# Performance work log

Measured on AMD Instinct MI355X. Metric: run time of the kernel, lower is better.

Reference implementation:

```python
import jax, jax.numpy as jnp
import numpy as np

NSITES = 64   # 2 * nphysical spin-orbital sites
BOND = 128    # MPS bond dimension D
BATCH = 16384 # sampled occupation configurations


def setup_inputs() -> dict:
    key = jax.random.key(0)
    k1, k2, k3, k4 = jax.random.split(key, 4)
    # Site tensors A[k, n] in R^{D x D}; scaled so chain products stay O(1).
    data = jax.random.normal(k1, (NSITES, 2, BOND, BOND), dtype=jnp.float32) / jnp.sqrt(jnp.float32(BOND))
    left = jax.random.normal(k2, (BOND,), dtype=jnp.float32)
    right = jax.random.normal(k3, (BOND,), dtype=jnp.float32)
    # Occupation-number vectors (0/1 per spin orbital).
    onstate = jax.random.randint(k4, (BATCH, NSITES), 0, 2, dtype=jnp.int32)
    # Orbital-ordering permutation (identity here).
    image2 = jnp.arange(NSITES, dtype=jnp.int32)
    return {"onstate": onstate, "data": data, "left": left, "right": right, "image2": image2}


def reference(onstate, data, left, right, image2):
    # Reorder physical indices per the stored orbital image: [B, NSITES]
    occ = onstate[:, image2]
    B = occ.shape[0]
    D = left.shape[0]
    v0 = jnp.broadcast_to(left, (B, D))  # left boundary, batched

    def step(v, xs):
        A, n = xs  # A: [2, D, D] site tensor, n: [B] occupations at this site
        # Contract with both quantum-number blocks, then select per sample
        # (equivalent to gathering the block indexed by the occupation).
        v_new = jnp.where((n == 1)[:, None], v @ A[1], v @ A[0])  # [B, D]
        return v_new, None

    vT, _ = jax.lax.scan(step, v0, (data, occ.T))
    return vT @ right  # amplitudes psi(n): [B]
```

## Files before the change

kernel.cpp:

```cpp
#include <hip/hip_runtime.h>
#include <hip/hip_bf16.h>

#define NS 64
#define NP 32
#define DIM 128
#define BATCH_N 16384

typedef float f32x4 __attribute__((ext_vector_type(4)));
typedef _Float16 f16x8 __attribute__((ext_vector_type(8)));
typedef __fp16 fp16x2 __attribute__((ext_vector_type(2)));
typedef unsigned int u32;
typedef unsigned long long u64;

__device__ __forceinline__ unsigned short f2h(float f) {
    _Float16 h = (_Float16)f;
    return __builtin_bit_cast(unsigned short, h);
}

__global__ __launch_bounds__(256)
void prep_pair_frags(const float* __restrict__ data,
                     unsigned short* __restrict__ afrag) {
    __shared__ float LA[2 * 32 * 129];
    __shared__ float LB[2 * 32 * 68];

    const int p   = blockIdx.x >> 3;
    const int kk  = (blockIdx.x >> 1) & 3;
    const int mh  = blockIdx.x & 1;
    const int tid = threadIdx.x;
    const int kgrp = tid >> 4;
    const int mgrp = tid & 15;

    const float* A0 = data + ((size_t)(2 * p) * 2 + 0) * DIM * DIM;
    const float* A1 = A0 + DIM * DIM;
    const float* B0 = data + ((size_t)(2 * p + 1) * 2 + 0) * DIM * DIM;
    const float* B1 = B0 + DIM * DIM;

    for (int c = tid; c < 32 * DIM; c += 256) {
        int kl = c >> 7, j = c & 127;
        float a0 = A0[(kk * 32 + kl) * DIM + j];
        float a1 = A1[(kk * 32 + kl) * DIM + j];
        LA[kl * 129 + j] = a0;
        LA[32 * 129 + kl * 129 + j] = a1 - a0;
    }

    float acc[2][2][2][4];
#pragma unroll
    for (int L = 0; L < 2; ++L)
#pragma unroll
        for (int R = 0; R < 2; ++R)
#pragma unroll
            for (int i = 0; i < 2; ++i)
#pragma unroll
                for (int mi = 0; mi < 4; ++mi) acc[L][R][i][mi] = 0.f;

    for (int ch = 0; ch < 4; ++ch) {
        __syncthreads();
        for (int c = tid; c < 32 * 64; c += 256) {
            int jl = c >> 6, ml = c & 63;
            float b0 = B0[(ch * 32 + jl) * DIM + mh * 64 + ml];
            float b1 = B1[(ch * 32 + jl) * DIM + mh * 64 + ml];
            LB[jl * 68 + ml] = b0;
            LB[32 * 68 + jl * 68 + ml] = b1 - b0;
        }
        __syncthreads();
#pragma unroll 2
        for (int jl = 0; jl < 32; ++jl) {
            int j = ch * 32 + jl;
            float la0[2], la1[2];
#pragma unroll
            for (int i = 0; i < 2; ++i) {
                la0[i] = LA[(kgrp * 2 + i) * 129 + j];
                la1[i] = LA[32 * 129 + (kgrp * 2 + i) * 129 + j];
            }
            f32x4 lb0 = *reinterpret_cast<const f32x4*>(&LB[jl * 68 + mgrp * 4]);
            f32x4 lb1 = *reinterpret_cast<const f32x4*>(&LB[32 * 68 + jl * 68 + mgrp * 4]);
#pragma unroll
            for (int i = 0; i < 2; ++i)
#pragma unroll
                for (int mi = 0; mi < 4; ++mi) {
                    acc[0][0][i][mi] += la0[i] * lb0[mi];
                    acc[1][0][i][mi] += la1[i] * lb0[mi];
                    acc[0][1][i][mi] += la0[i] * lb1[mi];
                    acc[1][1][i][mi] += la1[i] * lb1[mi];
                }
        }
    }

    const int H   = kk >> 1;
    const int kq  = kk & 1;
#pragma unroll
    for (int t = 0; t < 4; ++t) {
        int L = t & 1, R = t >> 1;
#pragma unroll
        for (int i = 0; i < 2; ++i)
#pragma unroll
            for (int mi = 0; mi < 4; ++mi) {
                int k = kk * 32 + kgrp * 2 + i;
                int m = mh * 64 + mgrp * 4 + mi;
                int mm = m >> 4;
                int lane = ((k & 31) >> 3) * 16 + (m & 15);
                int jj = k & 7;
                size_t idx =
                    ((size_t)((((p * 8 + mm) * 2 + H) * 4 + t) * 2 + kq)) * 512 +
                    lane * 8 + jj;
                afrag[idx] = f2h(acc[L][R][i][mi]);
            }
    }
}

__global__ void prep_bits(const int* __restrict__ onstate,
                          const int* __restrict__ image2,
                          u64* __restrict__ bits) {
    int r = blockIdx.x * blockDim.x + threadIdx.x;
    if (r >= BATCH_N) return;
    const int* row = onstate + (size_t)r * NS;
    u64 b = 0;
#pragma unroll 8
    for (int t = 0; t < NS; ++t) {
        b |= ((u64)(row[image2[t]] & 1)) << t;
    }
    bits[r] = b;
}

__global__ __launch_bounds__(512, 4)
void mps_pair(const unsigned short* __restrict__ afrag,
              const u64* __restrict__ occbits,
              const float* __restrict__ left,
              const float* __restrict__ right,
              float* __restrict__ out) {
    __shared__ unsigned short vlds[2][32 * DIM];
    __shared__ float red[32][33];

    const int tid  = threadIdx.x;
    const int wid  = tid >> 6;
    const int lane = tid & 63;
    const int li   = lane & 15;
    const int g    = lane >> 4;
    const int rbase = blockIdx.x * 32;

    u64 bits[2];
#pragma unroll
    for (int rg = 0; rg < 2; ++rg)
        bits[rg] = occbits[rbase + rg * 16 + li];

    const int voff0 = wid * 8192 + 2048 + lane * 8;
    const int voff1 = voff0 + 4096;

    u32 rdoff[2][4];
#pragma unroll
    for (int rg = 0; rg < 2; ++rg)
#pragma unroll
        for (int kk = 0; kk < 4; ++kk) {
            int r = rg * 16 + li;
            rdoff[rg][kk] =
                (u32)(r * 256 + kk * 64 + g * 16) ^ ((u32)(r & 7) << 4);
        }
    u32 wroff[2];
#pragma unroll
    for (int rg = 0; rg < 2; ++rg) {
        int r = rg * 16 + li;
        int mbase = wid * 16 + g * 4;
        wroff[rg] = (u32)(r * 256 + mbase * 2) ^ ((u32)(r & 7) << 4);
    }

    if (tid < 32 * 16) {
        int r  = tid >> 4;
        int kc = tid & 15;
        unsigned short tmp[8];
#pragma unroll
        for (int j = 0; j < 8; ++j) tmp[j] = f2h(left[kc * 8 + j]);
        u32 byte = (u32)(r * 256 + kc * 16) ^ ((u32)(r & 7) << 4);
        *reinterpret_cast<uint4*>(reinterpret_cast<char*>(&vlds[0][0]) + byte) =
            *reinterpret_cast<uint4*>(tmp);
    }
    __syncthreads();

    const f16x8 zf = {0, 0, 0, 0, 0, 0, 0, 0};

    f16x8 ft0[4][2], ft1[4][2];
    f32x4 acc[2];

#define ISSUE_CHUNK(FT, PB, VOFF)                                             \
    {                                                                         \
        _Pragma("unroll")                                                     \
        for (int t = 0; t < 4; ++t)                                           \
            _Pragma("unroll")                                                 \
            for (int kq = 0; kq < 2; ++kq)                                    \
                FT[t][kq] = *reinterpret_cast<const f16x8*>(                  \
                    (PB) + (VOFF) + (t * 1024 + kq * 512 - 2048));            \
    }

#define COMPUTE_HALF(P_, H_, FT)                                              \
    {                                                                         \
        const int p_ = (P_);                                                  \
        const char* vb = reinterpret_cast<const char*>(&vlds[p_ & 1][0]);     \
        __builtin_amdgcn_s_setprio(1);                                        \
        _Pragma("unroll")                                                     \
        for (int kq = 0; kq < 2; ++kq) {                                      \
            const int kk = 2 * (H_) + kq;                                     \
            f16x8 bfr[2];                                                     \
            _Pragma("unroll")                                                 \
            for (int rg = 0; rg < 2; ++rg)                                    \
                bfr[rg] =                                                     \
                    *reinterpret_cast<const f16x8*>(vb + rdoff[rg][kk]);      \
            _Pragma("unroll")                                                 \
            for (int rg = 0; rg < 2; ++rg) {                                  \
                bool m0 = (bits[rg] >> (2 * p_)) & 1;                         \
                bool m1 = (bits[rg] >> (2 * p_ + 1)) & 1;                     \
                f16x8 vb0  = m0 ? bfr[rg] : zf;                               \
                f16x8 vb1  = m1 ? bfr[rg] : zf;                               \
                f16x8 vb01 = m1 ? vb0 : zf;                                   \
                acc[rg] = __builtin_amdgcn_mfma_f32_16x16x32_f16(             \
                    FT[0][kq], bfr[rg], acc[rg], 0, 0, 0);                    \
                acc[rg] = __builtin_amdgcn_mfma_f32_16x16x32_f16(             \
                    FT[1][kq], vb0, acc[rg], 0, 0, 0);                        \
                acc[rg] = __builtin_amdgcn_mfma_f32_16x16x32_f16(             \
                    FT[2][kq], vb1, acc[rg], 0, 0, 0);                        \
                acc[rg] = __builtin_amdgcn_mfma_f32_16x16x32_f16(             \
                    FT[3][kq], vb01, acc[rg], 0, 0, 0);                       \
            }                                                                 \
        }                                                                     \
        __builtin_amdgcn_s_setprio(0);                                        \
    }

#define WRITE_PHASE(P_)                                                       \
    {                                                                         \
        const int p_ = (P_);                                                  \
        char* wb = reinterpret_cast<char*>(&vlds[(p_ + 1) & 1][0]);           \
        if (p_ < NP - 1) {                                                    \
            _Pragma("unroll")                                                 \
            for (int rg = 0; rg < 2; ++rg) {                                  \
                fp16x2 h01 = __builtin_amdgcn_cvt_pkrtz(acc[rg][0], acc[rg][1]); \
                fp16x2 h23 = __builtin_amdgcn_cvt_pkrtz(acc[rg][2], acc[rg][3]); \
                uint2 w = {__builtin_bit_cast(u32, h01),                      \
                           __builtin_bit_cast(u32, h23)};                     \
                *reinterpret_cast<uint2*>(wb + wroff[rg]) = w;                \
            }                                                                 \
            __syncthreads();                                                  \
        } else {                                                              \
            int mcol = wid * 16 + g * 4;                                      \
            const float4 rv = *reinterpret_cast<const float4*>(right + mcol); \
            _Pragma("unroll")                                                 \
            for (int rg = 0; rg < 2; ++rg) {                                  \
                float pv = acc[rg][0] * rv.x + acc[rg][1] * rv.y +            \
                           acc[rg][2] * rv.z + acc[rg][3] * rv.w;             \
                red[rg * 16 + li][wid * 4 + g] = pv;                          \
            }                                                                 \
            __syncthreads();                                                  \
            if (tid < 32) {                                                   \
                float ssum = 0.f;                                             \
                _Pragma("unroll")                                             \
                for (int i = 0; i < 32; ++i) ssum += red[tid][i];             \
                out[rbase + tid] = ssum;                                      \
            }                                                                 \
        }                                                                     \
    }

    ISSUE_CHUNK(ft0, afrag, voff0);
    for (int p = 0; p < NP; ++p) {
        const unsigned short* pb = afrag + ((size_t)p << 16);
        acc[0] = (f32x4){0.f, 0.f, 0.f, 0.f};
        acc[1] = (f32x4){0.f, 0.f, 0.f, 0.f};
        ISSUE_CHUNK(ft1, pb, voff1);
        COMPUTE_HALF(p, 0, ft0);
        if (p + 1 < NP) {
            const unsigned short* pbn = pb + 65536;
            ISSUE_CHUNK(ft0, pbn, voff0);
        }
        COMPUTE_HALF(p, 1, ft1);
        WRITE_PHASE(p);
    }

#undef ISSUE_CHUNK
#undef COMPUTE_HALF
#undef WRITE_PHASE
}

extern "C" void kernel_launch(void* const* d_in, const int* in_sizes, int n_in,
                              void* d_out, int out_size, void* d_ws, size_t ws_size,
                              hipStream_t stream) {
    const int*   onstate = (const int*)d_in[0];
    const float* data    = (const float*)d_in[1];
    const float* left    = (const float*)d_in[2];
    const float* right   = (const float*)d_in[3];
    const int*   image2  = (const int*)d_in[4];
    float* out = (float*)d_out;

    unsigned short* afrag = (unsigned short*)d_ws;
    u64* bits = (u64*)((char*)d_ws + (size_t)2097152 * sizeof(unsigned short));

    prep_pair_frags<<<256, 256, 0, stream>>>(data, afrag);
    prep_bits<<<64, 256, 0, stream>>>(onstate, image2, bits);
    mps_pair<<<512, 512, 0, stream>>>(afrag, bits, left, right, out);
}
```

Before: 118.7 us.

## Split K across wave pairs with 64-row blocks and LDS partial-sum exchange

The main kernel now runs 1024-thread blocks over 64 batch rows, up from 512 threads over 32. Each pair of waves splits the K dimension of the pair-site contraction, so each wave holds half as many A fragments in registers and reuses them across four row groups. The two half-K partial sums are exchanged through LDS, which adds extra barriers per pair step. This is meant to cut register pressure and global fragment traffic per row, at the cost of more synchronisation and a larger LDS footprint. It also switches fp16 conversion from packed round-toward-zero to round-to-nearest.

Result: slower. 245.8 us (+107.0%).

```diff
diff --git a/kernel.cpp b/kernel.cpp
--- a/kernel.cpp
+++ b/kernel.cpp
@@ -8,7 +8,6 @@
 
 typedef float f32x4 __attribute__((ext_vector_type(4)));
 typedef _Float16 f16x8 __attribute__((ext_vector_type(8)));
-typedef __fp16 fp16x2 __attribute__((ext_vector_type(2)));
 typedef unsigned int u32;
 typedef unsigned long long u64;
 
@@ -86,8 +85,8 @@
         }
     }
 
-    const int H   = kk >> 1;
-    const int kq  = kk & 1;
+    const int H  = kk >> 1;
+    const int kq = kk & 1;
 #pragma unroll
     for (int t = 0; t < 4; ++t) {
         int L = t & 1, R = t >> 1;
@@ -122,158 +121,163 @@
     bits[r] = b;
 }
 
-__global__ __launch_bounds__(512, 4)
+__global__ __launch_bounds__(1024, 4)
 void mps_pair(const unsigned short* __restrict__ afrag,
               const u64* __restrict__ occbits,
               const float* __restrict__ left,
               const float* __restrict__ right,
               float* __restrict__ out) {
-    __shared__ unsigned short vlds[2][32 * DIM];
-    __shared__ float red[32][33];
+    __shared__ char smem[49152];
 
     const int tid  = threadIdx.x;
     const int wid  = tid >> 6;
+    const int mt   = wid >> 1;
+    const int kh   = wid & 1;
     const int lane = tid & 63;
     const int li   = lane & 15;
     const int g    = lane >> 4;
-    const int rbase = blockIdx.x * 32;
-
-    u64 bits[2];
-#pragma unroll
-    for (int rg = 0; rg < 2; ++rg)
+    const int rbase = blockIdx.x * 64;
+
+    u64 bits[4];
+#pragma unroll
+    for (int rg = 0; rg < 4; ++rg)
         bits[rg] = occbits[rbase + rg * 16 + li];
 
-    const int voff0 = wid * 8192 + 2048 + lane * 8;
-    const int voff1 = voff0 + 4096;
+    const int voff = mt * 8192 + kh * 4096 + 2048 + lane * 8;
 
     u32 rdoff[2][4];
 #pragma unroll
-    for (int rg = 0; rg < 2; ++rg)
-#pragma unroll
-        for (int kk = 0; kk < 4; ++kk) {
+    for (int kq = 0; kq < 2; ++kq)
+#pragma unroll
+        for (int rg = 0; rg < 4; ++rg) {
             int r = rg * 16 + li;
-            rdoff[rg][kk] =
+            int kk = kh * 2 + kq;
+            rdoff[kq][rg] =
                 (u32)(r * 256 + kk * 64 + g * 16) ^ ((u32)(r & 7) << 4);
         }
+
+    const u32 exoff_w = (u32)((mt * 2 + kh) * 1024 + li * 64 + ((g ^ (li & 3)) << 4));
+    const u32 exoff_r = (u32)((mt * 2 + (kh ^ 1)) * 1024 + li * 64 + ((g ^ (li & 3)) << 4));
+
     u32 wroff[2];
 #pragma unroll
-    for (int rg = 0; rg < 2; ++rg) {
-        int r = rg * 16 + li;
-        int mbase = wid * 16 + g * 4;
-        wroff[rg] = (u32)(r * 256 + mbase * 2) ^ ((u32)(r & 7) << 4);
-    }
-
-    if (tid < 32 * 16) {
+    for (int R = 0; R < 2; ++R) {
+        int rgk = (kh ? 0 : 2) + R;
+        int r = rgk * 16 + li;
+        wroff[R] = (u32)(r * 256 + (mt * 16 + g * 4) * 2) ^ ((u32)(r & 7) << 4);
+    }
+
+    {
         int r  = tid >> 4;
         int kc = tid & 15;
         unsigned short tmp[8];
 #pragma unroll
         for (int j = 0; j < 8; ++j) tmp[j] = f2h(left[kc * 8 + j]);
         u32 byte = (u32)(r * 256 + kc * 16) ^ ((u32)(r & 7) << 4);
-        *reinterpret_cast<uint4*>(reinterpret_cast<char*>(&vlds[0][0]) + byte) =
-            *reinterpret_cast<uint4*>(tmp);
+        *reinterpret_cast<uint4*>(smem + byte) = *reinterpret_cast<uint4*>(tmp);
     }
     __syncthreads();
 
     const f16x8 zf = {0, 0, 0, 0, 0, 0, 0, 0};
-
-    f16x8 ft0[4][2], ft1[4][2];
-    f32x4 acc[2];
-
-#define ISSUE_CHUNK(FT, PB, VOFF)                                             \
+    f16x8 A[4][2];
+    float pvs[2] = {0.f, 0.f};
+
+#define ISSUE(P_)                                                             \
     {                                                                         \
+        const unsigned short* pb = afrag + (size_t)(P_)*65536 + voff;         \
         _Pragma("unroll")                                                     \
         for (int t = 0; t < 4; ++t)                                           \
             _Pragma("unroll")                                                 \
             for (int kq = 0; kq < 2; ++kq)                                    \
-                FT[t][kq] = *reinterpret_cast<const f16x8*>(                  \
-                    (PB) + (VOFF) + (t * 1024 + kq * 512 - 2048));            \
-    }
-
-#define COMPUTE_HALF(P_, H_, FT)                                              \
-    {                                                                         \
-        const int p_ = (P_);                                                  \
-        const char* vb = reinterpret_cast<const char*>(&vlds[p_ & 1][0]);     \
-        __builtin_amdgcn_s_setprio(1);                                        \
-        _Pragma("unroll")                                                     \
-        for (int kq = 0; kq < 2; ++kq) {                                      \
-            const int kk = 2 * (H_) + kq;                                     \
-            f16x8 bfr[2];                                                     \
-            _Pragma("unroll")                                                 \
-            for (int rg = 0; rg < 2; ++rg)                                    \
-                bfr[rg] =                                                     \
-                    *reinterpret_cast<const f16x8*>(vb + rdoff[rg][kk]);      \
-            _Pragma("unroll")                                                 \
-            for (int rg = 0; rg < 2; ++rg) {                                  \
-                bool m0 = (bits[rg] >> (2 * p_)) & 1;                         \
-                bool m1 = (bits[rg] >> (2 * p_ + 1)) & 1;                     \
-                f16x8 vb0  = m0 ? bfr[rg] : zf;                               \
-                f16x8 vb1  = m1 ? bfr[rg] : zf;                               \
-                f16x8 vb01 = m1 ? vb0 : zf;                                   \
-                acc[rg] = __builtin_amdgcn_mfma_f32_16x16x32_f16(             \
-                    FT[0][kq], bfr[rg], acc[rg], 0, 0, 0);                    \
-                acc[rg] = __builtin_amdgcn_mfma_f32_16x16x32_f16(             \
-                    FT[1][kq], vb0, acc[rg], 0, 0, 0);                        \
-                acc[rg] = __builtin_amdgcn_mfma_f32_16x16x32_f16(             \
-                    FT[2][kq], vb1, acc[rg], 0, 0, 0);                        \
-                acc[rg] = __builtin_amdgcn_mfma_f32_16x16x32_f16(             \
-                    FT[3][kq], vb01, acc[rg], 0, 0, 0);                       \
-            }                                                                 \
-        }                                                                     \
-        __builtin_amdgcn_s_setprio(0);                                        \
-    }
-
-#define WRITE_PHASE(P_)                                                       \
-    {                                                                         \
-        const int p_ = (P_);                                                  \
-        char* wb = reinterpret_cast<char*>(&vlds[(p_ + 1) & 1][0]);           \
-        if (p_ < NP - 1) {                                                    \
-            _Pragma("unroll")                                                 \
-            for (int rg = 0; rg < 2; ++rg) {                                  \
-                fp16x2 h01 = __builtin_amdgcn_cvt_pkrtz(acc[rg][0], acc[rg][1]); \
-                fp16x2 h23 = __builtin_amdgcn_cvt_pkrtz(acc[rg][2], acc[rg][3]); \
-                uint2 w = {__builtin_bit_cast(u32, h01),                      \
-                           __builtin_bit_cast(u32, h23)};                     \
-                *reinterpret_cast<uint2*>(wb + wroff[rg]) = w;                \
-            }                                                                 \
-            __syncthreads();                                                  \
-        } else {                                                              \
-            int mcol = wid * 16 + g * 4;                                      \
-            const float4 rv = *reinterpret_cast<const float4*>(right + mcol); \
-            _Pragma("unroll")                                                 \
-            for (int rg = 0; rg < 2; ++rg) {                                  \
-                float pv = acc[rg][0] * rv.x + acc[rg][1] * rv.y +            \
-                           acc[rg][2] * rv.z + acc[rg][3] * rv.w;             \
-                red[rg * 16 + li][wid * 4 + g] = pv;                          \
-            }                                                                 \
-            __syncthreads();                                                  \
-            if (tid < 32) {                                                   \
-                float ssum = 0.f;                                             \
-                _Pragma("unroll")                                             \
-                for (int i = 0; i < 32; ++i) ssum += red[tid][i];             \
-                out[rbase + tid] = ssum;                                      \
-            }                                                                 \
-        }                                                                     \
-    }
-
-    ISSUE_CHUNK(ft0, afrag, voff0);
+                A[t][kq] = *reinterpret_cast<const f16x8*>(                   \
+                    pb + (t * 1024 + kq * 512 - 2048));                       \
+    }
+
+    ISSUE(0);
     for (int p = 0; p < NP; ++p) {
-        const unsigned short* pb = afrag + ((size_t)p << 16);
-        acc[0] = (f32x4){0.f, 0.f, 0.f, 0.f};
-        acc[1] = (f32x4){0.f, 0.f, 0.f, 0.f};
-        ISSUE_CHUNK(ft1, pb, voff1);
-        COMPUTE_HALF(p, 0, ft0);
-        if (p + 1 < NP) {
-            const unsigned short* pbn = pb + 65536;
-            ISSUE_CHUNK(ft0, pbn, voff0);
-        }
-        COMPUTE_HALF(p, 1, ft1);
-        WRITE_PHASE(p);
-    }
-
-#undef ISSUE_CHUNK
-#undef COMPUTE_HALF
-#undef WRITE_PHASE
+        const char* vb = smem + (p & 1) * 16384;
+        char*       wb = smem + ((p + 1) & 1) * 16384;
+        char*       ex = smem + 32768;
+
+        f32x4 acc[4];
+#pragma unroll
+        for (int rg = 0; rg < 4; ++rg) acc[rg] = (f32x4){0.f, 0.f, 0.f, 0.f};
+
+        u32 mq[4];
+#pragma unroll
+        for (int rg = 0; rg < 4; ++rg) mq[rg] = (u32)(bits[rg] >> (2 * p));
+
+        __builtin_amdgcn_s_setprio(1);
+#pragma unroll
+        for (int kq = 0; kq < 2; ++kq) {
+            f16x8 bfr[4];
+#pragma unroll
+            for (int rg = 0; rg < 4; ++rg)
+                bfr[rg] = *reinterpret_cast<const f16x8*>(vb + rdoff[kq][rg]);
+#pragma unroll
+            for (int rg = 0; rg < 4; ++rg) {
+                bool m0 = mq[rg] & 1;
+                bool m1 = mq[rg] & 2;
+                f16x8 vb0  = m0 ? bfr[rg] : zf;
+                f16x8 vb1  = m1 ? bfr[rg] : zf;
+                f16x8 vb01 = m1 ? vb0 : zf;
+                acc[rg] = __builtin_amdgcn_mfma_f32_16x16x32_f16(
+                    A[0][kq], bfr[rg], acc[rg], 0, 0, 0);
+                acc[rg] = __builtin_amdgcn_mfma_f32_16x16x32_f16(
+                    A[1][kq], vb0, acc[rg], 0, 0, 0);
+                acc[rg] = __builtin_amdgcn_mfma_f32_16x16x32_f16(
+                    A[2][kq], vb1, acc[rg], 0, 0, 0);
+                acc[rg] = __builtin_amdgcn_mfma_f32_16x16x32_f16(
+                    A[3][kq], vb01, acc[rg], 0, 0, 0);
+            }
+        }
+        __builtin_amdgcn_s_setprio(0);
+
+        if (p + 1 < NP) ISSUE(p + 1);
+
+#pragma unroll
+        for (int R = 0; R < 2; ++R) {
+            const int wr_rg = kh * 2 + R;
+            const int kp_rg = (kh ^ 1) * 2 + R;
+            *reinterpret_cast<f32x4*>(ex + exoff_w) = acc[wr_rg];
+            __syncthreads();
+            f32x4 part = *reinterpret_cast<const f32x4*>(ex + exoff_r);
+            acc[kp_rg] += part;
+            if (p < NP - 1) {
+                u32 lo = ((u32)f2h(acc[kp_rg][1]) << 16) | f2h(acc[kp_rg][0]);
+                u32 hi = ((u32)f2h(acc[kp_rg][3]) << 16) | f2h(acc[kp_rg][2]);
+                uint2 w = {lo, hi};
+                *reinterpret_cast<uint2*>(wb + wroff[R]) = w;
+            } else {
+                int mcol = mt * 16 + g * 4;
+                const float4 rv = *reinterpret_cast<const float4*>(right + mcol);
+                pvs[R] = acc[kp_rg][0] * rv.x + acc[kp_rg][1] * rv.y +
+                         acc[kp_rg][2] * rv.z + acc[kp_rg][3] * rv.w;
+            }
+            __syncthreads();
+        }
+    }
+#undef ISSUE
+
+    char* red = smem + 32768;
+#pragma unroll
+    for (int R = 0; R < 2; ++R) {
+        float pv = pvs[R];
+        pv += __shfl_xor(pv, 16, 64);
+        pv += __shfl_xor(pv, 32, 64);
+        int rgk = (kh ? 0 : 2) + R;
+        int r = rgk * 16 + li;
+        if (g == 0)
+            *reinterpret_cast<float*>(red + (r * 8 + mt) * 4) = pv;
+    }
+    __syncthreads();
+    if (tid < 64) {
+        float s = 0.f;
+#pragma unroll
+        for (int i = 0; i < 8; ++i)
+            s += *reinterpret_cast<float*>(red + (tid * 8 + i) * 4);
+        out[rbase + tid] = s;
+    }
 }
 
 extern "C" void kernel_launch(void* const* d_in, const int* in_sizes, int n_in,
@@ -291,5 +295,5 @@
 
     prep_pair_frags<<<256, 256, 0, stream>>>(data, afrag);
     prep_bits<<<64, 256, 0, stream>>>(onstate, image2, bits);
-    mps_pair<<<512, 512, 0, stream>>>(afrag, bits, left, right, out);
-}
+    mps_pair<<<256, 1024, 0, stream>>>(afrag, bits, left, right, out);
+}
```
